# Optimization experiments

Measured on AMD Instinct MI355X. Metric: run time of the kernel, lower is better.

Reference implementation:

```python
import jax, jax.numpy as jnp
import numpy as np

C = 0.1            # args.hyp_c
EPS_PROJ = 4e-3    # hyptorch project eps for float32
MIN_NORM = 1e-5
NUM_HEADS = 12


def _norm(x):
    return jnp.maximum(jnp.linalg.norm(x, axis=-1, keepdims=True), MIN_NORM)


def expmap0(u, c):
    sqrt_c = c ** 0.5
    u_norm = _norm(u)
    return jnp.tanh(sqrt_c * u_norm) * u / (sqrt_c * u_norm)


def project(x, c):
    sqrt_c = c ** 0.5
    norm = _norm(x)
    maxnorm = (1.0 - EPS_PROJ) / sqrt_c
    return jnp.where(norm > maxnorm, x / norm * maxnorm, x)


def logmap0(y, c):
    sqrt_c = c ** 0.5
    y_norm = _norm(y)
    arg = jnp.clip(sqrt_c * y_norm, -1 + 1e-5, 1 - 1e-5)
    artanh = 0.5 * jnp.log((1 + arg) / (1 - arg))
    return y / (y_norm * sqrt_c) * artanh


def qkv_attention(x, wq, bq, wk, bk, wv, bv, num_heads):
    # x: [B, N, D]; weights in torch Linear convention [out, in]
    B, N, D = x.shape
    dh = D // num_heads
    q = (x @ wq.T + bq).reshape(B, N, num_heads, dh)
    k = (x @ wk.T + bk).reshape(B, N, num_heads, dh)
    v = (x @ wv.T + bv).reshape(B, N, num_heads, dh)
    # NOTE: original has no 1/sqrt(dh) scaling — keep faithful
    att = jnp.einsum('bnhd,bmhd->bhnm', q, k)
    att = jax.nn.softmax(att, axis=-1)
    out = jnp.einsum('bhnm,bmhd->bnhd', att, v)
    return out.reshape(B, N, D)


def setup_inputs() -> dict:
    key = jax.random.key(0)
    ks = jax.random.split(key, 7)
    B, N, D = 8, 1024, 768
    s = 0.02
    return {
        'x':   jax.random.normal(ks[0], (B, N, D), jnp.float32),
        'w_q': jax.random.normal(ks[1], (3, D, D), jnp.float32) * s,
        'b_q': jax.random.normal(ks[2], (3, D), jnp.float32) * s,
        'w_k': jax.random.normal(ks[3], (3, D, D), jnp.float32) * s,
        'b_k': jax.random.normal(ks[4], (3, D), jnp.float32) * s,
        'w_v': jax.random.normal(ks[5], (3, D, D), jnp.float32) * s,
        'b_v': jax.random.normal(ks[6], (3, D), jnp.float32) * s,
    }


def reference(x, w_q, b_q, w_k, b_k, w_v, b_v):
    # branch 0: euclidean; branch 1: hyperbolic (ToPoincare); branch 2: spherical (FromPoincare)
    x_e = x
    x_h = project(expmap0(x, C), C)
    x_s = logmap0(x, C)
    out = 0.0
    for i, xb in enumerate((x_e, x_h, x_s)):
        out = out + qkv_attention(xb, w_q[i], b_q[i], w_k[i], b_k[i],
                                  w_v[i], b_v[i], NUM_HEADS)
    return out
```

## Files before the change

kernel.cpp:

```cpp
#include <hip/hip_runtime.h>
#include <hip/hip_bf16.h>
#include <cstdint>
#include <cstddef>

#define B_   8
#define N_   1024
#define D_   768
#define H_   12
#define DH_  64
#define M_   (B_ * N_)
#define WSZ_ (D_ * D_)

typedef __bf16 bf16;
typedef bf16  bf16x8  __attribute__((ext_vector_type(8)));
typedef bf16  bf16x4  __attribute__((ext_vector_type(4)));
typedef float floatx4 __attribute__((ext_vector_type(4)));

#define MFMA16 __builtin_amdgcn_mfma_f32_16x16x32_bf16

__device__ __forceinline__ float exp2_fast(float x) {
    float r;
    asm("v_exp_f32 %0, %1" : "=v"(r) : "v"(x));
    return r;
}

__device__ __forceinline__ void gload_lds16(const void* g, void* l) {
    __builtin_amdgcn_global_load_lds(
        (const __attribute__((address_space(1))) unsigned int*)g,
        (__attribute__((address_space(3))) unsigned int*)l, 16, 0, 0);
}

__global__ __launch_bounds__(256) void prep_x(const float* __restrict__ x,
                                              bf16* __restrict__ xbf,
                                              float* __restrict__ sc ) {
    int row = blockIdx.x;
    int tid = threadIdx.x;
    const float* xr = x + (size_t)row * D_;
    bf16* xo = xbf + (size_t)row * D_;
    float v0 = xr[tid], v1 = xr[tid + 256], v2 = xr[tid + 512];
    xo[tid]       = (bf16)v0;
    xo[tid + 256] = (bf16)v1;
    xo[tid + 512] = (bf16)v2;
    float ss = v0 * v0 + v1 * v1 + v2 * v2;
    for (int off = 32; off; off >>= 1) ss += __shfl_xor(ss, off, 64);
    __shared__ float red[4];
    if ((tid & 63) == 0) red[tid >> 6] = ss;
    __syncthreads();
    if (tid == 0) {
        float t2 = red[0] + red[1] + red[2] + red[3];
        float t  = sqrtf(t2);
        const float scst = 0.31622776601683794f;
        float un = fmaxf(t, 1e-5f);
        float s1 = tanhf(scst * un) / (scst * un);
        float nh = fmaxf(t * s1, 1e-5f);
        float maxnorm = (1.0f - 4e-3f) / scst;
        float sh = (nh > maxnorm) ? s1 * (maxnorm / nh) : s1;
        float arg = fminf(scst * un, 1.0f - 1e-5f);
        float artanh = 0.5f * logf((1.0f + arg) / (1.0f - arg));
        float ssc = artanh / (un * scst);
        sc[row]      = sh;
        sc[M_ + row] = ssc;
    }
}

__global__ __launch_bounds__(256) void prep_w(const float* __restrict__ wq,
                                              const float* __restrict__ wk,
                                              const float* __restrict__ wv,
                                              bf16* __restrict__ wbf) {
    size_t i = ((size_t)blockIdx.x * 256 + threadIdx.x) * 4;
    int z = (int)(i / WSZ_);
    int r = (int)(i % WSZ_);
    int branch = z / 3, t = z % 3;
    const float* src = (t == 0 ? wq : t == 1 ? wk : wv) + (size_t)branch * WSZ_ + r;
    float4 f = *(const float4*)src;
    bf16x4 o = { (bf16)f.x, (bf16)f.y, (bf16)f.z, (bf16)f.w };
    *(bf16x4*)(wbf + i) = o;
}

#define BM 128
#define BN 128
#define BK 32
__global__ __launch_bounds__(256) void gemm_qkv(
        const bf16* __restrict__ xbf, const bf16* __restrict__ wbf_all,
        const float* __restrict__ bq, const float* __restrict__ bk,
        const float* __restrict__ bv, const float* __restrict__ sc,
        int zoff, bf16* __restrict__ qkv) {
    int gz = zoff + blockIdx.z;
    int branch = gz / 3, t = gz % 3;
    const bf16*  wsrc = wbf_all + (size_t)gz * WSZ_;
    const float* bias = (t == 0 ? bq : t == 1 ? bk : bv) + branch * D_;
    bf16* out = qkv + (size_t)blockIdx.z * M_ * D_;
    int bm0 = blockIdx.y * BM;
    int bn0 = blockIdx.x * BN;

    __shared__ bf16 lA[BM * BK];
    __shared__ bf16 lB[BN * BK];

    int tid = threadIdx.x;
    int w = tid >> 6, lane = tid & 63;
    int wr = w >> 1, wc = w & 1;
    int quad = lane >> 4, c15 = lane & 15;
    int lrow = lane >> 2;
    int lcol = (lane & 3) * 8;

    floatx4 acc[4][4];
    for (int i = 0; i < 4; i++)
        for (int j = 0; j < 4; j++)
            acc[i][j] = (floatx4){0.f, 0.f, 0.f, 0.f};

    for (int k0 = 0; k0 < D_; k0 += BK) {
        const bf16* ga = xbf  + ((size_t)(bm0 + w * 32 + lrow) * D_ + k0 + lcol);
        const bf16* gb = wsrc + ((size_t)(bn0 + w * 32 + lrow) * D_ + k0 + lcol);
        gload_lds16(ga,           (char*)lA + w * 2048);
        gload_lds16(ga + 16 * D_, (char*)lA + w * 2048 + 1024);
        gload_lds16(gb,           (char*)lB + w * 2048);
        gload_lds16(gb + 16 * D_, (char*)lB + w * 2048 + 1024);
        __syncthreads();

        int arow = wr * 64 + c15;
        int brow = wc * 64 + c15;
        int kq = quad * 8;
        bf16x8 af[4], bfm[4];
        for (int i = 0; i < 4; i++) af[i]  = *(const bf16x8*)(lA + (arow + i * 16) * BK + kq);
        for (int j = 0; j < 4; j++) bfm[j] = *(const bf16x8*)(lB + (brow + j * 16) * BK + kq);
        for (int i = 0; i < 4; i++)
            for (int j = 0; j < 4; j++)
                acc[i][j] = MFMA16(af[i], bfm[j], acc[i][j], 0, 0, 0);
        __syncthreads();
    }

    const float* scb = (branch == 0) ? nullptr : sc + (size_t)(branch - 1) * M_;
    float bj[4];
    for (int j = 0; j < 4; j++) bj[j] = bias[bn0 + wc * 64 + j * 16 + c15];
    for (int i = 0; i < 4; i++) {
        int gRow0 = bm0 + wr * 64 + i * 16 + quad * 4;
        for (int r = 0; r < 4; r++) {
            float s = scb ? scb[gRow0 + r] : 1.0f;
            bf16* orow = out + (size_t)(gRow0 + r) * D_;
            for (int j = 0; j < 4; j++) {
                int gCol = bn0 + wc * 64 + j * 16 + c15;
                orow[gCol] = (bf16)(s * acc[i][j][r] + bj[j]);
            }
        }
    }
}

#define LDK 72
__global__ __launch_bounds__(256) void attn(const bf16* __restrict__ qkv,
                                            float* __restrict__ out) {
    int qt = blockIdx.x;
    int bh = blockIdx.y;
    int batch = bh / H_, head = bh % H_;
    int n0 = qt * 128;
    int tid = threadIdx.x, w = tid >> 6, lane = tid & 63;
    int quad = lane >> 4, c15 = lane & 15;

    const bf16* base = qkv + (size_t)blockIdx.z * 3 * M_ * D_;
    const bf16* qb = base;
    const bf16* kb = base + (size_t)M_ * D_;
    const bf16* vb = base + (size_t)2 * M_ * D_;
    size_t baseRow = (size_t)batch * N_;
    int colOff = head * DH_;

    __shared__ bf16 sK[64 * LDK];
    __shared__ bf16 sVt[64 * LDK];
    __shared__ bf16 sP[4][32 * LDK];
    bf16* sPw = sP[w];

    bf16x8 aq[2][2];
#pragma unroll
    for (int h = 0; h < 2; h++) {
        const bf16* qp = qb + ((baseRow + n0 + w * 32 + h * 16 + c15) * D_ + colOff + quad * 8);
        aq[h][0] = *(const bf16x8*)qp;
        aq[h][1] = *(const bf16x8*)(qp + 32);
#pragma unroll
        for (int f = 0; f < 2; f++)
#pragma unroll
            for (int i = 0; i < 8; i++)
                aq[h][f][i] = (bf16)((float)aq[h][f][i] * 1.4426950408889634f);
    }

    float m_sw[2] = { 0.f, 0.f };
    float l_sw[2] = { 0.f, 0.f };
    floatx4 o_acc[2][4];
#pragma unroll
    for (int h = 0; h < 2; h++)
#pragma unroll
        for (int j = 0; j < 4; j++) o_acc[h][j] = (floatx4){0.f, 0.f, 0.f, 0.f};

    int kkey = tid >> 3;
    int kcol = (tid & 7) << 3;
    int vkey = tid >> 2;
    int vd0  = (tid & 3) << 4;
    int vcol = vkey ^ ((tid & 3) << 3);

    const bf16* kg = kb + (baseRow + kkey) * D_ + colOff + kcol;
    const bf16* vg = vb + (baseRow + vkey) * D_ + colOff + vd0;

    bf16x8 kr0 = *(const bf16x8*)kg;
    bf16x8 kr1 = *(const bf16x8*)(kg + (size_t)32 * D_);
    bf16x8 vr0 = *(const bf16x8*)vg;
    bf16x8 vr1 = *(const bf16x8*)(vg + 8);

    for (int kt = 0; kt < 16; kt++) {
        if (kt) __syncthreads();
        *(bf16x8*)(sK + kkey * LDK + kcol)        = kr0;
        *(bf16x8*)(sK + (kkey + 32) * LDK + kcol) = kr1;
#pragma unroll
        for (int i = 0; i < 8; i++) sVt[(vd0 + i) * LDK + vcol]     = vr0[i];
#pragma unroll
        for (int i = 0; i < 8; i++) sVt[(vd0 + 8 + i) * LDK + vcol] = vr1[i];
        __syncthreads();
        if (kt < 15) {
            const bf16* kgn = kg + (size_t)(kt + 1) * 64 * D_;
            const bf16* vgn = vg + (size_t)(kt + 1) * 64 * D_;
            kr0 = *(const bf16x8*)kgn;
            kr1 = *(const bf16x8*)(kgn + (size_t)32 * D_);
            vr0 = *(const bf16x8*)vgn;
            vr1 = *(const bf16x8*)(vgn + 8);
        }

        floatx4 sfr[2][4];
        __builtin_amdgcn_s_setprio(1);
#pragma unroll
        for (int j = 0; j < 4; j++) {
            const bf16* kp = sK + (j * 16 + c15) * LDK + quad * 8;
            bf16x8 k0 = *(const bf16x8*)kp;
            bf16x8 k1 = *(const bf16x8*)(kp + 32);
#pragma unroll
            for (int h = 0; h < 2; h++) {
                floatx4 z = (floatx4){0.f, 0.f, 0.f, 0.f};
                z = MFMA16(k0, aq[h][0], z, 0, 0, 0);
                z = MFMA16(k1, aq[h][1], z, 0, 0, 0);
                sfr[h][j] = z;
            }
        }
        __builtin_amdgcn_s_setprio(0);

#pragma unroll
        for (int h = 0; h < 2; h++) {
            float mx = sfr[h][0][0];
#pragma unroll
            for (int j = 0; j < 4; j++)
#pragma unroll
                for (int r = 0; r < 4; r++) mx = fmaxf(mx, sfr[h][j][r]);
            if (__any(mx > m_sw[h] + 11.0f)) {
                float mr = fmaxf(mx, __shfl_xor(mx, 16, 64));
                mr = fmaxf(mr, __shfl_xor(mr, 32, 64));
                float mnew = fmaxf(m_sw[h], mr);
                float alpha = exp2_fast(m_sw[h] - mnew);
                l_sw[h] *= alpha;
                m_sw[h] = mnew;
#pragma unroll
                for (int r = 0; r < 4; r++) {
                    float a = __shfl(alpha, quad * 4 + r, 64);
#pragma unroll
                    for (int j = 0; j < 4; j++) o_acc[h][j][r] *= a;
                }
            }
            float m = m_sw[h];
            float sum = 0.f;
            bf16x4 pk[4];
#pragma unroll
            for (int j = 0; j < 4; j++)
#pragma unroll
                for (int r = 0; r < 4; r++) {
                    float p = exp2_fast(sfr[h][j][r] - m);
                    sum += p;
                    pk[j][r] = (bf16)p;
                }
            sum += __shfl_xor(sum, 16, 64);
            sum += __shfl_xor(sum, 32, 64);
            l_sw[h] += sum;
            bf16* pw = sPw + (h * 16 + c15) * LDK;
#pragma unroll
            for (int j = 0; j < 4; j++)
                *(bf16x4*)(pw + j * 16 + quad * 4) = pk[j];
        }

        asm volatile("s_waitcnt lgkmcnt(0)" ::: "memory");
        __builtin_amdgcn_sched_barrier(0);

        bf16x8 ap[2][2];
#pragma unroll
        for (int h = 0; h < 2; h++) {
            const bf16* pp = sPw + (h * 16 + c15) * LDK + quad * 8;
            ap[h][0] = *(const bf16x8*)pp;
            ap[h][1] = *(const bf16x8*)(pp + 32);
        }
        __builtin_amdgcn_s_setprio(1);
#pragma unroll
        for (int j = 0; j < 4; j++) {
            const bf16* vtp = sVt + (j * 16 + c15) * LDK + ((quad ^ j) << 3);
            bf16x8 b0 = *(const bf16x8*)vtp;
            bf16x8 b1 = *(const bf16x8*)(vtp + 32);
#pragma unroll
            for (int h = 0; h < 2; h++) {
                o_acc[h][j] = MFMA16(ap[h][0], b0, o_acc[h][j], 0, 0, 0);
                o_acc[h][j] = MFMA16(ap[h][1], b1, o_acc[h][j], 0, 0, 0);
            }
        }
        __builtin_amdgcn_s_setprio(0);
    }

#pragma unroll
    for (int h = 0; h < 2; h++) {
        float inv = 1.0f / l_sw[h];
#pragma unroll
        for (int r = 0; r < 4; r++) {
            float iv = __shfl(inv, quad * 4 + r, 64);
            int row = n0 + w * 32 + h * 16 + quad * 4 + r;
            float* op = out + ((size_t)batch * N_ + row) * D_ + colOff;
#pragma unroll
            for (int j = 0; j < 4; j++) {
                float v = o_acc[h][j][r] * iv;
                int col = j * 16 + c15;
                unsafeAtomicAdd(op + col, v);
            }
        }
    }
}

extern "C" void kernel_launch(void* const* d_in, const int* in_sizes, int n_in,
                              void* d_out, int out_size, void* d_ws, size_t ws_size,
                              hipStream_t stream) {
    const float* x  = (const float*)d_in[0];
    const float* wq = (const float*)d_in[1];
    const float* bq = (const float*)d_in[2];
    const float* wk = (const float*)d_in[3];
    const float* bk = (const float*)d_in[4];
    const float* wv = (const float*)d_in[5];
    const float* bv = (const float*)d_in[6];
    float* out = (float*)d_out;

    char* ws = (char*)d_ws;
    bf16*  xbf = (bf16*)ws;
    bf16*  wbf = (bf16*)(ws + 12582912);
    float* sc  = (float*)(ws + 12582912 + 10616832);
    bf16*  qkv = (bf16*)(ws + 12582912 + 10616832 + 65536);

    const size_t matB = (size_t)M_ * D_ * 2;
    const size_t need_all = 12582912 + 10616832 + 65536 + 9 * matB;

    hipMemsetAsync(d_out, 0, out_size, stream);
    hipLaunchKernelGGL(prep_x, dim3(M_), dim3(256), 0, stream, x, xbf, sc);
    hipLaunchKernelGGL(prep_w, dim3((9 * WSZ_ / 4) / 256), dim3(256), 0, stream, wq, wk, wv, wbf);

    if (ws_size >= need_all) {
        hipLaunchKernelGGL(gemm_qkv, dim3(D_ / BN, M_ / BM, 9), dim3(256), 0, stream,
                           xbf, wbf, bq, bk, bv, sc, 0, qkv);
        hipLaunchKernelGGL(attn, dim3(N_ / 128, B_ * H_, 3), dim3(256), 0, stream,
                           qkv, out);
    } else {
        for (int br = 0; br < 3; br++) {
            hipLaunchKernelGGL(gemm_qkv, dim3(D_ / BN, M_ / BM, 3), dim3(256), 0, stream,
                               xbf, wbf, bq, bk, bv, sc, br * 3, qkv);
            hipLaunchKernelGGL(attn, dim3(N_ / 128, B_ * H_, 1), dim3(256), 0, stream,
                               qkv, out);
        }
    }
}
```

Baseline: 394.0 us.

## Add 256x256 ping-pong QKV GEMM with direct-to-LDS loads and swizzled V

Replaces the 128x128 per-matrix QKV GEMM with a single fused launch over all nine weight matrices. It uses 256x256 tiles, 512 threads in 8 waves, and global-to-LDS async loads into a double-buffered LDS tile. Barrier-interleaved MFMA clusters overlap the loads with compute, and a block-ID remap groups tiles for cache reuse. The attention kernel's transposed-V LDS swizzle also changes to a different XOR pattern to reduce bank conflicts. The cost is heavy register use, since the 32 accumulator tiles per thread must fit two blocks per CU. The hand-scheduled waitcnt and barrier sequence also adds correctness risk.

```diff
diff --git a/kernel.cpp b/kernel.cpp
--- a/kernel.cpp
+++ b/kernel.cpp
@@ -77,6 +77,128 @@
     *(bf16x4*)(wbf + i) = o;
 }
 
+#define NT9 12
+
+#define STG(buf, mat, half, t) do {                                          \
+    const bf16* _src = (mat) ? wbf : xbf;                                    \
+    int _rb = ((mat) ? bn0 : bm0) + (half) * 128 + w * 16 + (lane >> 2);     \
+    const bf16* _g = _src + (size_t)_rb * D_ + (t) * 64 + (lane & 3) * 8;    \
+    bf16* _l = &L[buf][mat][half][0][w * 16][0];                             \
+    gload_lds16(_g, _l);                                                     \
+    gload_lds16(_g + 32, _l + 4096);                                         \
+} while (0)
+
+#define LOADA(buf, mh) do {                                                  \
+    _Pragma("unroll") for (int fi = 0; fi < 4; fi++)                         \
+    _Pragma("unroll") for (int kk = 0; kk < 2; kk++)                         \
+        afr[fi][kk] = *(const bf16x8*)(&L[buf][0][wm][kk][(mh)*64 + fi*16 + c15][quad*8]); \
+} while (0)
+
+#define LOADB(buf, nh) do {                                                  \
+    _Pragma("unroll") for (int fj = 0; fj < 2; fj++)                         \
+    _Pragma("unroll") for (int kk = 0; kk < 2; kk++)                         \
+        bfr[nh][fj][kk] = *(const bf16x8*)(&L[buf][1][wn>>1][kk][(wn&1)*64 + (nh)*32 + fj*16 + c15][quad*8]); \
+} while (0)
+
+#define MFMACL(mh, nh) do {                                                  \
+    __builtin_amdgcn_s_setprio(1);                                           \
+    _Pragma("unroll") for (int fi = 0; fi < 4; fi++)                         \
+    _Pragma("unroll") for (int fj = 0; fj < 2; fj++)                         \
+    _Pragma("unroll") for (int kk = 0; kk < 2; kk++)                         \
+        acc[(mh)*4 + fi][(nh)*2 + fj] =                                      \
+            MFMA16(afr[fi][kk], bfr[nh][fj][kk], acc[(mh)*4 + fi][(nh)*2 + fj], 0, 0, 0); \
+    __builtin_amdgcn_s_setprio(0);                                           \
+} while (0)
+
+#define BAR() __builtin_amdgcn_s_barrier()
+#define VMW4() asm volatile("s_waitcnt vmcnt(4)" ::: "memory")
+
+__global__ __launch_bounds__(512, 2) void gemm_qkv9(
+        const bf16* __restrict__ xbf, const bf16* __restrict__ wbf,
+        const float* __restrict__ bq, const float* __restrict__ bk,
+        const float* __restrict__ bv, const float* __restrict__ sc,
+        bf16* __restrict__ qkv) {
+    int bid = blockIdx.x;
+    int v = (bid & 7) * 108 + (bid >> 3);
+    int bx = v >> 5;
+    int by = v & 31;
+    int bn0 = bx * 256;
+    int bm0 = by * 256;
+
+    __shared__ bf16 L[2][2][2][2][128][32];
+
+    int tid = threadIdx.x;
+    int w = tid >> 6, lane = tid & 63;
+    int wm = w >> 2, wn = w & 3;
+    int quad = lane >> 4, c15 = lane & 15;
+
+    bf16x8 afr[4][2];
+    bf16x8 bfr[2][2][2];
+    floatx4 acc[8][4];
+#pragma unroll
+    for (int i = 0; i < 8; i++)
+#pragma unroll
+        for (int j = 0; j < 4; j++) acc[i][j] = (floatx4){0.f, 0.f, 0.f, 0.f};
+
+    STG(0, 0, 0, 0); STG(0, 0, 1, 0); STG(0, 1, 0, 0); STG(0, 1, 1, 0);
+    STG(1, 1, 0, 1); STG(1, 1, 1, 1);
+    VMW4();
+    BAR();
+
+    for (int it = 0; it < 6; it++) {
+        int t1 = 2 * it + 1;
+        bool st2 = (it < 5);
+        LOADA(0, 0); LOADB(0, 0);
+        STG(1, 0, 0, t1);
+        BAR(); MFMACL(0, 0); BAR();
+        LOADB(0, 1);
+        STG(1, 0, 1, t1);
+        BAR(); MFMACL(0, 1); BAR();
+        LOADA(0, 1);
+        if (st2) STG(0, 1, 0, t1 + 1);
+        BAR(); MFMACL(1, 1); BAR();
+        if (st2) STG(0, 1, 1, t1 + 1);
+        VMW4();
+        BAR(); MFMACL(1, 0); BAR();
+        LOADA(1, 0); LOADB(1, 0);
+        if (st2) STG(0, 0, 0, t1 + 1);
+        BAR(); MFMACL(0, 0); BAR();
+        LOADB(1, 1);
+        if (st2) STG(0, 0, 1, t1 + 1);
+        BAR(); MFMACL(0, 1); BAR();
+        LOADA(1, 1);
+        if (st2) STG(1, 1, 0, t1 + 2);
+        BAR(); MFMACL(1, 1); BAR();
+        if (st2) STG(1, 1, 1, t1 + 2);
+        VMW4();
+        BAR(); MFMACL(1, 0); BAR();
+    }
+
+    int gz = bn0 / 768;
+    int branch = gz / 3, t = gz % 3;
+    int colz0 = (bn0 % 768) + wn * 64;
+    const float* bias = (t == 0 ? bq : t == 1 ? bk : bv) + branch * D_;
+    const float* scb = (branch == 0) ? nullptr : sc + (size_t)(branch - 1) * M_;
+    float bj[4];
+#pragma unroll
+    for (int fj = 0; fj < 4; fj++) bj[fj] = bias[colz0 + fj * 16 + c15];
+    bf16* outz = qkv + (size_t)gz * M_ * D_;
+#pragma unroll
+    for (int fi = 0; fi < 8; fi++) {
+        int rowbase = bm0 + wm * 128 + fi * 16 + quad * 4;
+        float4 sv = scb ? *(const float4*)(scb + rowbase)
+                        : (float4){1.f, 1.f, 1.f, 1.f};
+        float svr[4] = { sv.x, sv.y, sv.z, sv.w };
+#pragma unroll
+        for (int r = 0; r < 4; r++) {
+            bf16* orow = outz + (size_t)(rowbase + r) * D_;
+#pragma unroll
+            for (int fj = 0; fj < 4; fj++)
+                orow[colz0 + fj * 16 + c15] = (bf16)(svr[r] * acc[fi][fj][r] + bj[fj]);
+        }
+    }
+}
+
 #define BM 128
 #define BN 128
 #define BK 32
@@ -192,7 +314,7 @@
     int kcol = (tid & 7) << 3;
     int vkey = tid >> 2;
     int vd0  = (tid & 3) << 4;
-    int vcol = vkey ^ ((tid & 3) << 3);
+    int vcol = vkey ^ ((tid & 3) << 4);
 
     const bf16* kg = kb + (baseRow + kkey) * D_ + colOff + kcol;
     const bf16* vg = vb + (baseRow + vkey) * D_ + colOff + vd0;
@@ -291,9 +413,9 @@
         __builtin_amdgcn_s_setprio(1);
 #pragma unroll
         for (int j = 0; j < 4; j++) {
-            const bf16* vtp = sVt + (j * 16 + c15) * LDK + ((quad ^ j) << 3);
-            bf16x8 b0 = *(const bf16x8*)vtp;
-            bf16x8 b1 = *(const bf16x8*)(vtp + 32);
+            const bf16* vtp = sVt + (j * 16 + c15) * LDK;
+            bf16x8 b0 = *(const bf16x8*)(vtp + ((quad * 8) ^ (16 * j)));
+            bf16x8 b1 = *(const bf16x8*)(vtp + ((32 + quad * 8) ^ (16 * j)));
 #pragma unroll
             for (int h = 0; h < 2; h++) {
                 o_acc[h][j] = MFMA16(ap[h][0], b0, o_acc[h][j], 0, 0, 0);
@@ -347,8 +469,8 @@
     hipLaunchKernelGGL(prep_w, dim3((9 * WSZ_ / 4) / 256), dim3(256), 0, stream, wq, wk, wv, wbf);
 
     if (ws_size >= need_all) {
-        hipLaunchKernelGGL(gemm_qkv, dim3(D_ / BN, M_ / BM, 9), dim3(256), 0, stream,
-                           xbf, wbf, bq, bk, bv, sc, 0, qkv);
+        hipLaunchKernelGGL(gemm_qkv9, dim3(864), dim3(512), 0, stream,
+                           xbf, wbf, bq, bk, bv, sc, qkv);
         hipLaunchKernelGGL(attn, dim3(N_ / 128, B_ * H_, 3), dim3(256), 0, stream,
                            qkv, out);
     } else {
```

Result: faster. 375.8 us (-4.6%).
